# Kernel tuning notes

Measured on AMD Instinct MI355X. Metric: run time of the kernel, lower is better.

Reference implementation:

```python
import jax, jax.numpy as jnp
import numpy as np

N_NODES = 50000
N_EDGES = 400000
N_GRAPHS = 256
NUM_TYPES = 200
EMB = 64
HID = 128
HEADS = 4
GDIM = 256  # graph_embed_dim
NUM_CLASSES = 20
EPS = 1e-5
NEG_SLOPE = 0.2


def _gat_conv(h, src, dst, W, a_src, a_dst, bias, heads, out_c, concat):
    """PyG GATConv (with self-loops already appended to src/dst)."""
    n = h.shape[0]
    x = (h @ W.T).reshape(n, heads, out_c)                       # [N,H,C]
    al_s = jnp.einsum('nhc,hc->nh', x, a_src)                    # [N,H]
    al_d = jnp.einsum('nhc,hc->nh', x, a_dst)
    e = jax.nn.leaky_relu(al_s[src] + al_d[dst], NEG_SLOPE)      # [E',H]
    # segment softmax over destination node
    e_max = jax.ops.segment_max(e, dst, num_segments=n)
    e_exp = jnp.exp(e - e_max[dst])
    denom = jax.ops.segment_sum(e_exp, dst, num_segments=n)
    alpha = e_exp / denom[dst]                                   # [E',H]
    out = jax.ops.segment_sum(alpha[:, :, None] * x[src], dst, num_segments=n)  # [N,H,C]
    out = out.reshape(n, heads * out_c) if concat else out.mean(axis=1)
    return out + bias


def _batchnorm(h, gamma, beta):
    # training-mode BatchNorm1d over node dim (biased variance, as torch)
    m = h.mean(axis=0)
    v = jnp.mean((h - m) ** 2, axis=0)
    return (h - m) * jax.lax.rsqrt(v + EPS) * gamma + beta


def setup_inputs() -> dict:
    key = jax.random.key(0)
    ks = jax.random.split(key, 32)
    s = 0.1
    inp = {
        'x': jax.random.randint(ks[0], (N_NODES,), 0, NUM_TYPES),
        'edge_index': jax.random.randint(ks[1], (2, N_EDGES), 0, N_NODES),
        'depth': jax.random.uniform(ks[2], (N_NODES,), jnp.float32),
        'batch': jnp.sort(jax.random.randint(ks[3], (N_NODES,), 0, N_GRAPHS)),
        'emb_table': jax.random.normal(ks[4], (NUM_TYPES, EMB), jnp.float32) * s,
        'depth_w': jax.random.normal(ks[5], (EMB, 1), jnp.float32) * s,
        'depth_b': jnp.zeros((EMB,), jnp.float32),
        'W0': jax.random.normal(ks[6], (HEADS * HID, EMB), jnp.float32) * s,
        'as0': jax.random.normal(ks[7], (HEADS, HID), jnp.float32) * s,
        'ad0': jax.random.normal(ks[8], (HEADS, HID), jnp.float32) * s,
        'b0': jnp.zeros((HEADS * HID,), jnp.float32),
        'g0': jnp.ones((HEADS * HID,), jnp.float32),
        'be0': jnp.zeros((HEADS * HID,), jnp.float32),
        'W1': jax.random.normal(ks[9], (HEADS * HID, HEADS * HID), jnp.float32) * s,
        'as1': jax.random.normal(ks[10], (HEADS, HID), jnp.float32) * s,
        'ad1': jax.random.normal(ks[11], (HEADS, HID), jnp.float32) * s,
        'b1': jnp.zeros((HEADS * HID,), jnp.float32),
        'g1': jnp.ones((HEADS * HID,), jnp.float32),
        'be1': jnp.zeros((HEADS * HID,), jnp.float32),
        # layer 2: 512 -> 128, 1 head, no concat
        'W2': jax.random.normal(ks[12], (GDIM // 2, HEADS * HID), jnp.float32) * s,
        'as2': jax.random.normal(ks[13], (1, GDIM // 2), jnp.float32) * s,
        'ad2': jax.random.normal(ks[14], (1, GDIM // 2), jnp.float32) * s,
        'b2': jnp.zeros((GDIM // 2,), jnp.float32),
        'g2': jnp.ones((GDIM // 2,), jnp.float32),
        'be2': jnp.zeros((GDIM // 2,), jnp.float32),
        # classifier: 256 -> 256 -> 20
        'cw1': jax.random.normal(ks[15], (GDIM, 2 * (GDIM // 2)), jnp.float32) * s,
        'cb1': jnp.zeros((GDIM,), jnp.float32),
        'cw2': jax.random.normal(ks[16], (NUM_CLASSES, GDIM), jnp.float32) * s,
        'cb2': jnp.zeros((NUM_CLASSES,), jnp.float32),
    }
    return inp


def reference(x, edge_index, depth, batch, emb_table, depth_w, depth_b,
              W0, as0, ad0, b0, g0, be0,
              W1, as1, ad1, b1, g1, be1,
              W2, as2, ad2, b2, g2, be2,
              cw1, cb1, cw2, cb2):
    n = x.shape[0]
    # node features: type embedding + depth projection
    h = emb_table[x] + (depth[:, None] @ depth_w.T + depth_b)    # [N,64]
    # add self-loops once (PyG GATConv default add_self_loops=True)
    loop = jnp.arange(n)
    src = jnp.concatenate([edge_index[0], loop])
    dst = jnp.concatenate([edge_index[1], loop])
    layers = [
        (W0, as0, ad0, b0, g0, be0, HEADS, HID, True),
        (W1, as1, ad1, b1, g1, be1, HEADS, HID, True),
        (W2, as2, ad2, b2, g2, be2, 1, GDIM // 2, False),
    ]
    for (W, a_s, a_d, b, g, be, heads, out_c, concat) in layers:
        h = _gat_conv(h, src, dst, W, a_s, a_d, b, heads, out_c, concat)
        h = _batchnorm(h, g, be)
        h = jax.nn.elu(h)
        # dropout: eval mode -> identity
    # global mean / max pooling per graph
    ones = jnp.ones((n,), h.dtype)
    counts = jax.ops.segment_sum(ones, batch, num_segments=N_GRAPHS)
    h_mean = jax.ops.segment_sum(h, batch, num_segments=N_GRAPHS) / jnp.maximum(counts, 1.0)[:, None]
    h_max = jax.ops.segment_max(h, batch, num_segments=N_GRAPHS)
    emb = jnp.concatenate([h_mean, h_max], axis=-1)              # [G,256]
    # classifier (dropout off in eval)
    hidden = jax.nn.relu(emb @ cw1.T + cb1)
    return hidden @ cw2.T + cb2                                  # [G,20]
```

## Files before the change

### kernel.cpp

```cpp
#include <hip/hip_runtime.h>

#define N_NODES 50000
#define N_PAD 50048
#define NBY 391
#define N_EDGES 400000
#define EP (N_EDGES + N_NODES)
#define N_GRAPHS 256
#define EMB 64
#define HID 128
#define HEADS 4
#define GDIM 256
#define NUM_CLASSES 20
#define EPS_BN 1e-5f
#define NEG_SLOPE 0.2f
#define NB_AGG 2048

typedef __attribute__((ext_vector_type(4))) float f32x4;
typedef _Float16 h8 __attribute__((ext_vector_type(8)));
typedef _Float16 h4 __attribute__((ext_vector_type(4)));
typedef _Float16 h2 __attribute__((ext_vector_type(2)));

#define GLD(g, l)                                                              \
    __builtin_amdgcn_global_load_lds(                                          \
        (const __attribute__((address_space(1))) void*)(g),                    \
        (__attribute__((address_space(3))) void*)(l), 16, 0, 0)

__global__ void k_deg(const int* __restrict__ ei, int* __restrict__ deg) {
    int e = blockIdx.x * blockDim.x + threadIdx.x;
    if (e >= EP) return;
    int dst = (e < N_EDGES) ? ei[N_EDGES + e] : (e - N_EDGES);
    atomicAdd(&deg[dst], 1);
}

__global__ void k_scanA(const int* __restrict__ deg, int* __restrict__ incl, int* __restrict__ bsums) {
    __shared__ int sh[1024];
    int t = threadIdx.x;
    int i = blockIdx.x * 1024 + t;
    int v = (i < N_NODES) ? deg[i] : 0;
    int xv = v;
    sh[t] = xv;
    __syncthreads();
    for (int off = 1; off < 1024; off <<= 1) {
        int y = (t >= off) ? sh[t - off] : 0;
        __syncthreads();
        xv += y;
        sh[t] = xv;
        __syncthreads();
    }
    if (i < N_NODES) incl[i] = xv;
    if (t == 1023) bsums[blockIdx.x] = xv;
}

__global__ void k_scanC(const int* __restrict__ incl, const int* __restrict__ deg,
                        const int* __restrict__ bsums, int* __restrict__ offs) {
    int i = blockIdx.x * blockDim.x + threadIdx.x;
    int b = i >> 10;
    int add = 0;
    for (int k = 0; k < b; k++) add += bsums[k];
    if (i < N_NODES) offs[i] = incl[i] - deg[i] + add;
    if (i == 0) offs[N_NODES] = EP;
}

__global__ void k_scatter(const int* __restrict__ ei, const int* __restrict__ offs,
                          int* __restrict__ cnt, int* __restrict__ csr) {
    int e = blockIdx.x * blockDim.x + threadIdx.x;
    if (e >= EP) return;
    int src, dst;
    if (e < N_EDGES) { src = ei[e]; dst = ei[N_EDGES + e]; }
    else { src = e - N_EDGES; dst = src; }
    int pos = atomicAdd(&cnt[dst], 1);
    csr[offs[dst] + pos] = src;
}

__device__ __forceinline__ void cvt1(const float* __restrict__ in, _Float16* __restrict__ o, int i) {
    int f = i * 4;
    float4 v = *(const float4*)(in + f);
    h4 r;
    r[0] = (_Float16)v.x; r[1] = (_Float16)v.y; r[2] = (_Float16)v.z; r[3] = (_Float16)v.w;
    *(h4*)(o + f) = r;
}

__global__ __launch_bounds__(256) void k_setup(const float* __restrict__ W0, const float* __restrict__ as0,
                                               const float* __restrict__ ad0, const float* __restrict__ W1,
                                               const float* __restrict__ W2,
                                               _Float16* __restrict__ W0f, _Float16* __restrict__ W1f,
                                               _Float16* __restrict__ W2f,
                                               float* __restrict__ wtil,
                                               float* __restrict__ bn0, float* __restrict__ bn1,
                                               float* __restrict__ bn2) {
    int b = blockIdx.x, t = threadIdx.x;
    if (b < 256) {
        cvt1(W1, W1f, b * 256 + t);
    } else if (b < 288) {
        cvt1(W0, W0f, (b - 256) * 256 + t);
    } else if (b < 352) {
        cvt1(W2, W2f, (b - 288) * 256 + t);
    } else if (b == 352) {
        int h = t >> 6, k = t & 63;
        float ss = 0.f, sd = 0.f;
        for (int c = 0; c < 128; c++) {
            float w = W0[(size_t)(h * 128 + c) * 64 + k];
            ss += w * as0[h * 128 + c];
            sd += w * ad0[h * 128 + c];
        }
        wtil[t] = ss;
        wtil[256 + t] = sd;
    } else {
        for (int i = t; i < 1024; i += 256) { bn0[i] = 0.f; bn1[i] = 0.f; bn2[i] = 0.f; }
    }
}

__global__ __launch_bounds__(256) void k_node_al0(const int* __restrict__ x,
                                                  const float* __restrict__ depth,
                                                  const float* __restrict__ emb_table,
                                                  const float* __restrict__ dw,
                                                  const float* __restrict__ db,
                                                  const float* __restrict__ wtil,
                                                  const int* __restrict__ batch,
                                                  _Float16* __restrict__ h16,
                                                  float* __restrict__ als, float* __restrict__ ald,
                                                  int* __restrict__ goffs) {
    int wid = threadIdx.x >> 6, lane = threadIdx.x & 63;
    int n = blockIdx.x * 4 + wid;
    if (n >= N_NODES) return;
    float v = emb_table[x[n] * EMB + lane] + depth[n] * dw[lane] + db[lane];
    h16[(size_t)n * 64 + lane] = (_Float16)v;
#pragma unroll
    for (int h = 0; h < 4; h++) {
        float ps = v * wtil[h * 64 + lane];
        float pd = v * wtil[256 + h * 64 + lane];
        for (int off = 32; off; off >>= 1) {
            ps += __shfl_xor(ps, off);
            pd += __shfl_xor(pd, off);
        }
        if (lane == 0) { als[n * 4 + h] = ps; ald[n * 4 + h] = pd; }
    }
    if (lane == 0) {
        int b = batch[n];
        int bp = (n == 0) ? -1 : batch[n - 1];
        for (int g = bp + 1; g <= b; g++) goffs[g] = n;
        if (n == N_NODES - 1) {
            for (int g = b + 1; g <= N_GRAPHS; g++) goffs[g] = N_NODES;
        }
    }
}

__global__ __launch_bounds__(256) void k_bnelu(_Float16* __restrict__ a,
                                               const float* __restrict__ sums,
                                               const float* __restrict__ gamma,
                                               const float* __restrict__ beta) {
    const int lane = threadIdx.x & 63;
    const int wid = threadIdx.x >> 6;
    const int c0 = lane * 8;
    const float invN = 1.f / (float)N_NODES;
    float sc[8], sh[8];
#pragma unroll
    for (int k = 0; k < 8; k += 4) {
        float4 s4 = *(const float4*)(sums + c0 + k);
        float4 q4 = *(const float4*)(sums + 512 + c0 + k);
        float4 g4 = *(const float4*)(gamma + c0 + k);
        float4 b4 = *(const float4*)(beta + c0 + k);
        float m, v;
        m = s4.x * invN; v = q4.x * invN - m * m;
        sc[k + 0] = g4.x * __frsqrt_rn(v + EPS_BN); sh[k + 0] = b4.x - m * sc[k + 0];
        m = s4.y * invN; v = q4.y * invN - m * m;
        sc[k + 1] = g4.y * __frsqrt_rn(v + EPS_BN); sh[k + 1] = b4.y - m * sc[k + 1];
        m = s4.z * invN; v = q4.z * invN - m * m;
        sc[k + 2] = g4.z * __frsqrt_rn(v + EPS_BN); sh[k + 2] = b4.z - m * sc[k + 2];
        m = s4.w * invN; v = q4.w * invN - m * m;
        sc[k + 3] = g4.w * __frsqrt_rn(v + EPS_BN); sh[k + 3] = b4.w - m * sc[k + 3];
    }
    const int stride = gridDim.x * 8;
    for (int n = (blockIdx.x * 4 + wid) * 2; n < N_NODES; n += stride) {
        _Float16* p0 = a + (size_t)n * 512 + c0;
        _Float16* p1 = p0 + 512;
        h8 v0 = *(h8*)p0;
        h8 v1 = *(h8*)p1;
        h8 o0, o1;
#pragma unroll
        for (int k = 0; k < 8; k++) {
            float x0 = (float)v0[k] * sc[k] + sh[k];
            x0 = x0 > 0.f ? x0 : expm1f(x0);
            o0[k] = (_Float16)x0;
            float x1 = (float)v1[k] * sc[k] + sh[k];
            x1 = x1 > 0.f ? x1 : expm1f(x1);
            o1[k] = (_Float16)x1;
        }
        *(h8*)p0 = o0;
        *(h8*)p1 = o1;
    }
}

__global__ __launch_bounds__(256) void k_agg0(const _Float16* __restrict__ h16,
                                              const float* __restrict__ als,
                                              const float* __restrict__ ald_g,
                                              const int* __restrict__ offs,
                                              const int* __restrict__ csr,
                                              _Float16* __restrict__ outh) {
    const int lane = threadIdx.x & 63;
    const int wwid = threadIdx.x >> 6;
    const int q = lane >> 4, l = lane & 15;
    const int gw = blockIdx.x * 4 + wwid;
    const int stride = gridDim.x * 16;
    for (int n = gw * 4 + q; n < N_NODES; n += stride) {
        int s0 = offs[n], s1 = offs[n + 1];
        float aldl = (l < 4) ? ald_g[n * 4 + l] : 0.f;
        float acc[4][4] = {};
        float den[4] = {};
        int e = s0;
        for (; e + 4 <= s1; e += 4) {
            int srcA = csr[e], srcB = csr[e + 1];
            int srcC = csr[e + 2], srcD = csr[e + 3];
            float wA = 0.f, wB = 0.f, wC = 0.f, wD = 0.f;
            if (l < 4) {
                float a1 = als[srcA * 4 + l] + aldl;
                a1 = a1 > 0.f ? a1 : NEG_SLOPE * a1;
                wA = expf(a1);
                float a2 = als[srcB * 4 + l] + aldl;
                a2 = a2 > 0.f ? a2 : NEG_SLOPE * a2;
                wB = expf(a2);
                float a3 = als[srcC * 4 + l] + aldl;
                a3 = a3 > 0.f ? a3 : NEG_SLOPE * a3;
                wC = expf(a3);
                float a4 = als[srcD * 4 + l] + aldl;
                a4 = a4 > 0.f ? a4 : NEG_SLOPE * a4;
                wD = expf(a4);
            }
            h4 vA = *(const h4*)(h16 + (size_t)srcA * 64 + l * 4);
            h4 vB = *(const h4*)(h16 + (size_t)srcB * 64 + l * 4);
            h4 vC = *(const h4*)(h16 + (size_t)srcC * 64 + l * 4);
            h4 vD = *(const h4*)(h16 + (size_t)srcD * 64 + l * 4);
            float vA0 = (float)vA[0], vA1 = (float)vA[1], vA2 = (float)vA[2], vA3 = (float)vA[3];
            float vB0 = (float)vB[0], vB1 = (float)vB[1], vB2 = (float)vB[2], vB3 = (float)vB[3];
            float vC0 = (float)vC[0], vC1 = (float)vC[1], vC2 = (float)vC[2], vC3 = (float)vC[3];
            float vD0 = (float)vD[0], vD1 = (float)vD[1], vD2 = (float)vD[2], vD3 = (float)vD[3];
#pragma unroll
            for (int h = 0; h < 4; h++) {
                float whA = __shfl(wA, q * 16 + h);
                float whB = __shfl(wB, q * 16 + h);
                float whC = __shfl(wC, q * 16 + h);
                float whD = __shfl(wD, q * 16 + h);
                den[h] += (whA + whB) + (whC + whD);
                acc[h][0] += whA * vA0 + whB * vB0 + whC * vC0 + whD * vD0;
                acc[h][1] += whA * vA1 + whB * vB1 + whC * vC1 + whD * vD1;
                acc[h][2] += whA * vA2 + whB * vB2 + whC * vC2 + whD * vD2;
                acc[h][3] += whA * vA3 + whB * vB3 + whC * vC3 + whD * vD3;
            }
        }
        for (; e < s1; e++) {
            int src = csr[e];
            float w = 0.f;
            if (l < 4) {
                float a1 = als[src * 4 + l] + aldl;
                a1 = a1 > 0.f ? a1 : NEG_SLOPE * a1;
                w = expf(a1);
            }
            h4 v = *(const h4*)(h16 + (size_t)src * 64 + l * 4);
            float v0 = (float)v[0], v1 = (float)v[1], v2 = (float)v[2], v3 = (float)v[3];
#pragma unroll
            for (int h = 0; h < 4; h++) {
                float wh = __shfl(w, q * 16 + h);
                den[h] += wh;
                acc[h][0] += wh * v0;
                acc[h][1] += wh * v1;
                acc[h][2] += wh * v2;
                acc[h][3] += wh * v3;
            }
        }
#pragma unroll
        for (int h = 0; h < 4; h++) {
            float id = 1.f / den[h];
            h4 hv;
            hv[0] = (_Float16)(acc[h][0] * id);
            hv[1] = (_Float16)(acc[h][1] * id);
            hv[2] = (_Float16)(acc[h][2] * id);
            hv[3] = (_Float16)(acc[h][3] * id);
            *(h4*)(outh + (size_t)n * 256 + h * 64 + l * 4) = hv;
        }
    }
}

__global__ __launch_bounds__(256) void k_gemm0h(const _Float16* __restrict__ A,
                                                const _Float16* __restrict__ W,
                                                const float* __restrict__ bias,
                                                _Float16* __restrict__ outA,
                                                float* __restrict__ bnacc) {
    __shared__ h8 sA[2][512], sW[2][512];
    const int nbx = gridDim.x;
    const int d = blockIdx.y * nbx + blockIdx.x;
    const int by = (d / (8 * nbx)) * 8 + (d & 7);
    const int bx = (d >> 3) % nbx;
    if (by >= NBY) return;
    const int hd = bx;
    const int t = threadIdx.x;
    const int lane = t & 63;
    const int wid = t >> 6;
    const int wm = wid >> 1, wn = wid & 1;
    const int r0 = by * 128;
    const int l15 = lane & 15, quad = lane >> 4;
    f32x4 acc[4][4] = {};
    auto stage = [&](int buf, int kb) {
#pragma unroll
        for (int r = 0; r < 2; r++) {
            int c = r * 256 + t;
            int row = c >> 2, q = c & 3;
            size_t gA = ((size_t)(r0 + row) * 256 + hd * 64 + kb) * 2 + q * 16;
            size_t gW = ((size_t)(hd * 128 + row) * 64 + kb) * 2 + q * 16;
            GLD((const char*)A + gA, (char*)&sA[buf][0] + c * 16);
            GLD((const char*)W + gW, (char*)&sW[buf][0] + c * 16);
        }
    };
    stage(0, 0);
    __syncthreads();
#pragma unroll
    for (int ki = 0; ki < 2; ki++) {
        int cur = ki & 1;
        if (ki + 1 < 2) stage(cur ^ 1, (ki + 1) * 32);
        h8 a[4], w[4];
#pragma unroll
        for (int i = 0; i < 4; i++) {
            a[i] = sA[cur][(wm * 64 + i * 16 + l15) * 4 + quad];
            w[i] = sW[cur][(wn * 64 + i * 16 + l15) * 4 + quad];
        }
#pragma unroll
        for (int i = 0; i < 4; i++)
#pragma unroll
            for (int j = 0; j < 4; j++)
                acc[i][j] = __builtin_amdgcn_mfma_f32_16x16x32_f16(a[i], w[j], acc[i][j], 0, 0, 0);
        __syncthreads();
    }
    float colsum[4] = {}, colsq[4] = {};
#pragma unroll
    for (int i = 0; i < 4; i++) {
        int gr = r0 + wm * 64 + i * 16 + quad * 4;
#pragma unroll
        for (int j = 0; j < 4; j++) {
            int gc = hd * 128 + wn * 64 + j * 16 + l15;
            float bv = bias[gc];
#pragma unroll
            for (int rg = 0; rg < 4; rg++) {
                int rr = gr + rg;
                if (rr < N_NODES) {
                    float o = acc[i][j][rg] + bv;
                    outA[(size_t)rr * 512 + gc] = (_Float16)o;
                    colsum[j] += o;
                    colsq[j] += o * o;
                }
            }
        }
    }
#pragma unroll
    for (int j = 0; j < 4; j++) {
        colsum[j] += __shfl_xor(colsum[j], 16);
        colsum[j] += __shfl_xor(colsum[j], 32);
        colsq[j] += __shfl_xor(colsq[j], 16);
        colsq[j] += __shfl_xor(colsq[j], 32);
    }
    float* sS = (float*)&sA[0][0];
    float* sQ = (float*)&sW[0][0];
    __syncthreads();
    if (quad == 0) {
#pragma unroll
        for (int j = 0; j < 4; j++) {
            int c = wn * 64 + j * 16 + l15;
            sS[c * 2 + wm] = colsum[j];
            sQ[c * 2 + wm] = colsq[j];
        }
    }
    __syncthreads();
    if (t < 128) {
        atomicAdd(bnacc + hd * 128 + t, sS[t * 2] + sS[t * 2 + 1]);
        atomicAdd(bnacc + 512 + hd * 128 + t, sQ[t * 2] + sQ[t * 2 + 1]);
    }
}

__global__ __launch_bounds__(256) void k_gemm_mfma(const _Float16* __restrict__ A,
                                                   const _Float16* __restrict__ W,
                                                   const float* __restrict__ a_src,
                                                   const float* __restrict__ a_dst,
                                                   float* __restrict__ als_g,
                                                   float* __restrict__ ald_g,
                                                   _Float16* __restrict__ out,
                                                   int K, int M, int heads) {
    __shared__ h8 sA[2][512], sW[2][512];
    const int nbx = gridDim.x;
    const int d = blockIdx.y * nbx + blockIdx.x;
    const int by = (d / (8 * nbx)) * 8 + (d & 7);
    const int bx = (d >> 3) % nbx;
    if (by >= NBY) return;
    const int t = threadIdx.x;
    const int lane = t & 63;
    const int wid = t >> 6;
    const int wm = wid >> 1, wn = wid & 1;
    const int r0 = by * 128, c0 = bx * 128;
    const int l15 = lane & 15, quad = lane >> 4;
    f32x4 acc[4][4] = {};
    auto stage = [&](int buf, int kb) {
#pragma unroll
        for (int r = 0; r < 2; r++) {
            int c = r * 256 + t;
            int row = c >> 2, q = c & 3;
            size_t gA = ((size_t)(r0 + row) * K + kb) * 2 + q * 16;
            size_t gW = ((size_t)(c0 + row) * K + kb) * 2 + q * 16;
            GLD((const char*)A + gA, (char*)&sA[buf][0] + c * 16);
            GLD((const char*)W + gW, (char*)&sW[buf][0] + c * 16);
        }
    };
    stage(0, 0);
    __syncthreads();
    const int nkb = K >> 5;
    for (int ki = 0; ki < nkb; ki++) {
        int cur = ki & 1;
        if (ki + 1 < nkb) stage(cur ^ 1, (ki + 1) * 32);
        h8 a[4], w[4];
#pragma unroll
        for (int i = 0; i < 4; i++) {
            a[i] = sA[cur][(wm * 64 + i * 16 + l15) * 4 + quad];
            w[i] = sW[cur][(wn * 64 + i * 16 + l15) * 4 + quad];
        }
#pragma unroll
        for (int i = 0; i < 4; i++)
#pragma unroll
            for (int j = 0; j < 4; j++)
                acc[i][j] = __builtin_amdgcn_mfma_f32_16x16x32_f16(a[i], w[j], acc[i][j], 0, 0, 0);
        __syncthreads();
    }
#pragma unroll
    for (int i = 0; i < 4; i++) {
        int gr = r0 + wm * 64 + i * 16 + quad * 4;
#pragma unroll
        for (int j = 0; j < 4; j++) {
            int gc = c0 + wn * 64 + j * 16 + l15;
#pragma unroll
            for (int rg = 0; rg < 4; rg++) {
                int rr = gr + rg;
                if (rr < N_NODES) out[(size_t)rr * M + gc] = (_Float16)acc[i][j][rg];
            }
        }
    }
    const int hd = bx;
    float ps[4][4] = {}, pd[4][4] = {};
#pragma unroll
    for (int j = 0; j < 4; j++) {
        int ch = wn * 64 + j * 16 + l15;
        float av = a_src[hd * 128 + ch];
        float dv = a_dst[hd * 128 + ch];
#pragma unroll
        for (int i = 0; i < 4; i++)
#pragma unroll
            for (int rg = 0; rg < 4; rg++) {
                ps[i][rg] += acc[i][j][rg] * av;
                pd[i][rg] += acc[i][j][rg] * dv;
            }
    }
#pragma unroll
    for (int m = 1; m < 16; m <<= 1)
#pragma unroll
        for (int i = 0; i < 4; i++)
#pragma unroll
            for (int rg = 0; rg < 4; rg++) {
                ps[i][rg] += __shfl_xor(ps[i][rg], m);
                pd[i][rg] += __shfl_xor(pd[i][rg], m);
            }
    float* sS = (float*)&sA[0][0];
    float* sD = (float*)&sW[0][0];
    if (l15 == 0) {
#pragma unroll
        for (int i = 0; i < 4; i++)
#pragma unroll
            for (int rg = 0; rg < 4; rg++) {
                int ri = wm * 64 + i * 16 + quad * 4 + rg;
                sS[ri * 2 + wn] = ps[i][rg];
                sD[ri * 2 + wn] = pd[i][rg];
            }
    }
    __syncthreads();
    if (t < 128) {
        int row = r0 + t;
        if (row < N_NODES) {
            als_g[row * heads + hd] = sS[t * 2] + sS[t * 2 + 1];
            ald_g[row * heads + hd] = sD[t * 2] + sD[t * 2 + 1];
        }
    }
}

__global__ __launch_bounds__(256) void k_agg512(const _Float16* __restrict__ xf,
                                                const float* __restrict__ als,
                                                const float* __restrict__ ald_g,
                                                const int* __restrict__ offs,
                                                const int* __restrict__ csr,
                                                const float* __restrict__ bias,
                                                _Float16* __restrict__ out16,
                                                float* __restrict__ bnacc) {
    __shared__ float pool[4][1024];
    const int wid = threadIdx.x >> 6, lane = threadIdx.x & 63;
    int* s_src = (int*)&pool[wid][0];
    float* s_w = &pool[wid][64];
    const int gw = blockIdx.x * 4 + wid;
    const int nw = gridDim.x * 4;
    const int hh = lane >> 4;
    const int c0 = lane * 8;
    float bias8[8];
#pragma unroll
    for (int k = 0; k < 8; k++) bias8[k] = bias[c0 + k];
    float bns[8] = {}, bnq[8] = {};
    for (int n = gw; n < N_NODES; n += nw) {
        int s0 = offs[n], s1 = offs[n + 1];
        float4 aldv = *(const float4*)(ald_g + n * 4);
        float a[8] = {};
        float den = 0.f;
        for (int base = s0; base < s1; base += 64) {
            int j = base + lane;
            int srcj = 0;
            float4 alv = make_float4(0.f, 0.f, 0.f, 0.f);
            if (j < s1) {
                srcj = csr[j];
                alv = *(const float4*)(als + srcj * 4);
            }
            float e0 = alv.x + aldv.x; e0 = e0 > 0.f ? e0 : NEG_SLOPE * e0;
            float e1 = alv.y + aldv.y; e1 = e1 > 0.f ? e1 : NEG_SLOPE * e1;
            float e2 = alv.z + aldv.z; e2 = e2 > 0.f ? e2 : NEG_SLOPE * e2;
            float e3 = alv.w + aldv.w; e3 = e3 > 0.f ? e3 : NEG_SLOPE * e3;
            s_src[lane] = srcj;
            s_w[0 * 64 + lane] = expf(e0);
            s_w[1 * 64 + lane] = expf(e1);
            s_w[2 * 64 + lane] = expf(e2);
            s_w[3 * 64 + lane] = expf(e3);
            int cend = min(64, s1 - base);
            int e = 0;
            for (; e + 8 <= cend; e += 8) {
                h8 v[8];
                float w[8];
#pragma unroll
                for (int u = 0; u < 8; u++) {
                    v[u] = *(const h8*)(xf + (size_t)s_src[e + u] * 512 + c0);
                    w[u] = s_w[hh * 64 + e + u];
                }
#pragma unroll
                for (int u = 0; u < 8; u++) {
                    den += w[u];
#pragma unroll
                    for (int k = 0; k < 8; k++) a[k] += w[u] * (float)v[u][k];
                }
            }
            for (; e + 2 <= cend; e += 2) {
                h8 vA = *(const h8*)(xf + (size_t)s_src[e] * 512 + c0);
                h8 vB = *(const h8*)(xf + (size_t)s_src[e + 1] * 512 + c0);
                float wA = s_w[hh * 64 + e], wB = s_w[hh * 64 + e + 1];
                den += wA + wB;
#pragma unroll
                for (int k = 0; k < 8; k++) a[k] += wA * (float)vA[k] + wB * (float)vB[k];
            }
            if (e < cend) {
                h8 v = *(const h8*)(xf + (size_t)s_src[e] * 512 + c0);
                float w = s_w[hh * 64 + e];
                den += w;
#pragma unroll
                for (int k = 0; k < 8; k++) a[k] += w * (float)v[k];
            }
        }
        float id = 1.f / den;
        h8 ov;
#pragma unroll
        for (int k = 0; k < 8; k++) {
            float o = a[k] * id + bias8[k];
            ov[k] = (_Float16)o;
            bns[k] += o;
            bnq[k] += o * o;
        }
        *(h8*)(out16 + (size_t)n * 512 + c0) = ov;
    }
#pragma unroll
    for (int k = 0; k < 8; k++) {
        pool[wid][c0 + k] = bns[k];
        pool[wid][512 + c0 + k] = bnq[k];
    }
    __syncthreads();
    for (int t = threadIdx.x; t < 1024; t += 256)
        atomicAdd(bnacc + t, pool[0][t] + pool[1][t] + pool[2][t] + pool[3][t]);
}

__global__ __launch_bounds__(256) void k_agg128(const _Float16* __restrict__ xf,
                                                const float* __restrict__ als,
                                                const float* __restrict__ ald_g,
                                                const int* __restrict__ offs,
                                                const int* __restrict__ csr,
                                                const float* __restrict__ bias,
                                                _Float16* __restrict__ out_h,
                                                float* __restrict__ bnacc) {
    __shared__ float pool[4][256];
    const int wid = threadIdx.x >> 6, lane = threadIdx.x & 63;
    int* s_src = (int*)&pool[wid][0];
    float* s_w = &pool[wid][64];
    const int gw = blockIdx.x * 4 + wid;
    const int nw = gridDim.x * 4;
    const int c = lane * 2;
    const float2 biasv = *(const float2*)(bias + c);
    float bns0 = 0.f, bns1 = 0.f, bnq0 = 0.f, bnq1 = 0.f;
    for (int n = gw; n < N_NODES; n += nw) {
        int s0 = offs[n], s1 = offs[n + 1];
        float aldv = ald_g[n];
        float ax = 0.f, ay = 0.f, den = 0.f;
        for (int base = s0; base < s1; base += 64) {
            int j = base + lane;
            int srcj = 0;
            float alv = 0.f;
            if (j < s1) { srcj = csr[j]; alv = als[srcj]; }
            float e0 = alv + aldv;
            e0 = e0 > 0.f ? e0 : NEG_SLOPE * e0;
            s_src[lane] = srcj;
            s_w[lane] = expf(e0);
            int cend = min(64, s1 - base);
            int e = 0;
            for (; e + 8 <= cend; e += 8) {
                h2 v[8];
                float w[8];
#pragma unroll
                for (int u = 0; u < 8; u++) {
                    v[u] = *(const h2*)(xf + (size_t)s_src[e + u] * 128 + c);
                    w[u] = s_w[e + u];
                }
#pragma unroll
                for (int u = 0; u < 8; u++) {
                    den += w[u];
                    ax += w[u] * (float)v[u][0];
                    ay += w[u] * (float)v[u][1];
                }
            }
            for (; e < cend; e++) {
                h2 v = *(const h2*)(xf + (size_t)s_src[e] * 128 + c);
                float w = s_w[e];
                den += w;
                ax += w * (float)v[0];
                ay += w * (float)v[1];
            }
        }
        float id = 1.f / den;
        float ox = ax * id + biasv.x;
        float oy = ay * id + biasv.y;
        h2 oh;
        oh[0] = (_Float16)ox;
        oh[1] = (_Float16)oy;
        *(h2*)(out_h + (size_t)n * 128 + c) = oh;
        bns0 += ox; bnq0 += ox * ox;
        bns1 += oy; bnq1 += oy * oy;
    }
    pool[wid][c] = bns0; pool[wid][c + 1] = bns1;
    pool[wid][128 + c] = bnq0; pool[wid][128 + c + 1] = bnq1;
    __syncthreads();
    {
        int t = threadIdx.x;
        atomicAdd(bnacc + t, pool[0][t] + pool[1][t] + pool[2][t] + pool[3][t]);
    }
}

__global__ __launch_bounds__(256) void k_poolclassify(const _Float16* __restrict__ C,
                                                      const float* __restrict__ bnsums,
                                                      const float* __restrict__ gamma,
                                                      const float* __restrict__ beta,
                                                      const int* __restrict__ goffs,
                                                      const float* __restrict__ cw1, const float* __restrict__ cb1,
                                                      const float* __restrict__ cw2, const float* __restrict__ cb2,
                                                      float* __restrict__ out) {
    __shared__ float er[256];
    __shared__ float red[256];
    int g = blockIdx.x, t = threadIdx.x;
    int c = t & 127, half = t >> 7;
    const float invN = 1.f / (float)N_NODES;
    float m = bnsums[c] * invN;
    float var = bnsums[128 + c] * invN - m * m;
    float sc = gamma[c] * __frsqrt_rn(var + EPS_BN);
    float sh = beta[c] - m * sc;
    int s = goffs[g], e = goffs[g + 1];
    float sum = 0.f, mx = -INFINITY;
    for (int n = s + half; n < e; n += 2) {
        float x = (float)C[(size_t)n * 128 + c] * sc + sh;
        x = x > 0.f ? x : expm1f(x);
        sum += x;
        mx = fmaxf(mx, x);
    }
    red[t] = sum;
    __syncthreads();
    float sumT = red[c] + red[128 + c];
    __syncthreads();
    red[t] = mx;
    __syncthreads();
    float mxT = fmaxf(red[c], red[128 + c]);
    int cnt = e - s;
    if (half == 0) {
        er[c] = sumT / (float)max(cnt, 1);
        er[128 + c] = mxT;
    }
    __syncthreads();
    float acc = cb1[t];
    for (int k = 0; k < 256; k++) acc += er[k] * cw1[t * 256 + k];
    __syncthreads();
    red[t] = fmaxf(acc, 0.f);
    __syncthreads();
    if (t < NUM_CLASSES) {
        float o = cb2[t];
        for (int k = 0; k < 256; k++) o += red[k] * cw2[t * 256 + k];
        out[g * NUM_CLASSES + t] = o;
    }
}

extern "C" void kernel_launch(void* const* d_in, const int* in_sizes, int n_in,
                              void* d_out, int out_size, void* d_ws, size_t ws_size,
                              hipStream_t stream) {
    (void)in_sizes; (void)n_in; (void)out_size; (void)ws_size;
    const int* x = (const int*)d_in[0];
    const int* ei = (const int*)d_in[1];
    const float* depth = (const float*)d_in[2];
    const int* batch = (const int*)d_in[3];
    const float* emb_table = (const float*)d_in[4];
    const float* depth_w = (const float*)d_in[5];
    const float* depth_b = (const float*)d_in[6];
    const float* W0 = (const float*)d_in[7];
    const float* as0 = (const float*)d_in[8];
    const float* ad0 = (const float*)d_in[9];
    const float* b0 = (const float*)d_in[10];
    const float* g0 = (const float*)d_in[11];
    const float* be0 = (const float*)d_in[12];
    const float* W1 = (const float*)d_in[13];
    const float* as1 = (const float*)d_in[14];
    const float* ad1 = (const float*)d_in[15];
    const float* b1 = (const float*)d_in[16];
    const float* g1 = (const float*)d_in[17];
    const float* be1 = (const float*)d_in[18];
    const float* W2 = (const float*)d_in[19];
    const float* as2 = (const float*)d_in[20];
    const float* ad2 = (const float*)d_in[21];
    const float* b2 = (const float*)d_in[22];
    const float* g2 = (const float*)d_in[23];
    const float* be2 = (const float*)d_in[24];
    const float* cw1 = (const float*)d_in[25];
    const float* cb1 = (const float*)d_in[26];
    const float* cw2 = (const float*)d_in[27];
    const float* cb2 = (const float*)d_in[28];
    float* out = (float*)d_out;

    size_t off = 0;
    char* base = (char*)d_ws;
    auto carve = [&](size_t bytes) -> void* {
        void* p = base + off;
        off += (bytes + 255) & ~(size_t)255;
        return p;
    };
    float* B = (float*)carve((size_t)N_NODES * 512 * 2);
    _Float16* A16 = (_Float16*)carve((size_t)N_PAD * 512 * 2);
    _Float16* W0f = (_Float16*)carve((size_t)512 * 64 * 2);
    _Float16* W1f = (_Float16*)carve((size_t)512 * 512 * 2);
    _Float16* W2f = (_Float16*)carve((size_t)128 * 512 * 2);
    float* als = (float*)carve((size_t)N_NODES * HEADS * 4);
    float* ald = (float*)carve((size_t)N_NODES * HEADS * 4);
    float* bn0 = (float*)carve(1024 * 4);
    float* bn1 = (float*)carve(1024 * 4);
    float* bn2 = (float*)carve(1024 * 4);
    float* wtil = (float*)carve(512 * 4);
    int* deg = (int*)carve((size_t)2 * N_NODES * 4);
    int* cnt = deg + N_NODES;
    int* incl = (int*)carve((size_t)N_NODES * 4);
    int* offs = (int*)carve((size_t)(N_NODES + 1) * 4);
    int* bsums = (int*)carve(64 * 4);
    int* csr = (int*)carve((size_t)EP * 4);
    int* goffs = (int*)carve((size_t)(N_GRAPHS + 1) * 4);

    _Float16* h16 = (_Float16*)B;
    _Float16* hth = (_Float16*)((char*)B + (size_t)N_NODES * 64 * 2);
    _Float16* Bh = (_Float16*)B;
    _Float16* C = (_Float16*)A16;

    const int TPB = 256;
    int gbN = (N_NODES + TPB - 1) / TPB;
    int gbE = (EP + TPB - 1) / TPB;
    int nbScan = (N_NODES + 1023) / 1024;
    int gbNode4 = (N_NODES + 3) / 4;
    dim3 g512(4, 392);
    dim3 g128(1, 391);

    hipMemsetAsync(deg, 0, (size_t)2 * N_NODES * 4, stream);
    k_setup<<<354, TPB, 0, stream>>>(W0, as0, ad0, W1, W2, W0f, W1f, W2f, wtil, bn0, bn1, bn2);
    k_deg<<<gbE, TPB, 0, stream>>>(ei, deg);
    k_scanA<<<nbScan, 1024, 0, stream>>>(deg, incl, bsums);
    k_scanC<<<gbN, TPB, 0, stream>>>(incl, deg, bsums, offs);
    k_scatter<<<gbE, TPB, 0, stream>>>(ei, offs, cnt, csr);

    k_node_al0<<<gbNode4, TPB, 0, stream>>>(x, depth, emb_table, depth_w, depth_b, wtil,
                                            batch, h16, als, ald, goffs);
    k_agg0<<<NB_AGG, TPB, 0, stream>>>(h16, als, ald, offs, csr, hth);
    k_gemm0h<<<g512, TPB, 0, stream>>>(hth, W0f, b0, A16, bn0);
    k_bnelu<<<2048, TPB, 0, stream>>>(A16, bn0, g0, be0);
    k_gemm_mfma<<<g512, TPB, 0, stream>>>(A16, W1f, as1, ad1, als, ald, Bh, 512, 512, HEADS);
    k_agg512<<<NB_AGG, TPB, 0, stream>>>(Bh, als, ald, offs, csr, b1, A16, bn1);
    k_bnelu<<<2048, TPB, 0, stream>>>(A16, bn1, g1, be1);
    k_gemm_mfma<<<g128, TPB, 0, stream>>>(A16, W2f, as2, ad2, als, ald, Bh, 512, 128, 1);
    k_agg128<<<NB_AGG, TPB, 0, stream>>>(Bh, als, ald, offs, csr, b2, C, bn2);
    k_poolclassify<<<N_GRAPHS, TPB, 0, stream>>>(C, bn2, g2, be2, goffs, cw1, cb1, cw2, cb2, out);
}
```

Measured before the change: 581.4 us.

## Fuse BatchNorm+ELU into GEMM A-tile staging and fold deg memset into setup

Removes the two standalone BN+ELU passes over the 50000x512 fp16 activations. The BN scale and shift are now computed per block into shared memory, and the normalisation and ELU are applied while the A tile is loaded through registers into LDS inside the MFMA GEMM. A is loaded with register loads instead of async global-to-LDS loads, and the transform is interleaved after the MFMAs. The deg/cnt memset is folded into extra blocks of the setup kernel. The cost is that the ELU is recomputed for every column block (4x for layer 1) and the A load path is no longer asynchronous.

```diff
diff --git a/kernel.cpp b/kernel.cpp
--- a/kernel.cpp
+++ b/kernel.cpp
@@ -87,7 +87,8 @@
                                                _Float16* __restrict__ W2f,
                                                float* __restrict__ wtil,
                                                float* __restrict__ bn0, float* __restrict__ bn1,
-                                               float* __restrict__ bn2) {
+                                               float* __restrict__ bn2,
+                                               int* __restrict__ deg) {
     int b = blockIdx.x, t = threadIdx.x;
     if (b < 256) {
         cvt1(W1, W1f, b * 256 + t);
@@ -105,8 +106,11 @@
         }
         wtil[t] = ss;
         wtil[256 + t] = sd;
+    } else if (b == 353) {
+        for (int i = t; i < 1024; i += 256) { bn0[i] = 0.f; bn1[i] = 0.f; bn2[i] = 0.f; }
     } else {
-        for (int i = t; i < 1024; i += 256) { bn0[i] = 0.f; bn1[i] = 0.f; bn2[i] = 0.f; }
+        int i4 = (b - 354) * 256 + t;
+        if (i4 < 25000) ((int4*)deg)[i4] = make_int4(0, 0, 0, 0);
     }
 }
 
@@ -142,52 +146,6 @@
         if (n == N_NODES - 1) {
             for (int g = b + 1; g <= N_GRAPHS; g++) goffs[g] = N_NODES;
         }
-    }
-}
-
-__global__ __launch_bounds__(256) void k_bnelu(_Float16* __restrict__ a,
-                                               const float* __restrict__ sums,
-                                               const float* __restrict__ gamma,
-                                               const float* __restrict__ beta) {
-    const int lane = threadIdx.x & 63;
-    const int wid = threadIdx.x >> 6;
-    const int c0 = lane * 8;
-    const float invN = 1.f / (float)N_NODES;
-    float sc[8], sh[8];
-#pragma unroll
-    for (int k = 0; k < 8; k += 4) {
-        float4 s4 = *(const float4*)(sums + c0 + k);
-        float4 q4 = *(const float4*)(sums + 512 + c0 + k);
-        float4 g4 = *(const float4*)(gamma + c0 + k);
-        float4 b4 = *(const float4*)(beta + c0 + k);
-        float m, v;
-        m = s4.x * invN; v = q4.x * invN - m * m;
-        sc[k + 0] = g4.x * __frsqrt_rn(v + EPS_BN); sh[k + 0] = b4.x - m * sc[k + 0];
-        m = s4.y * invN; v = q4.y * invN - m * m;
-        sc[k + 1] = g4.y * __frsqrt_rn(v + EPS_BN); sh[k + 1] = b4.y - m * sc[k + 1];
-        m = s4.z * invN; v = q4.z * invN - m * m;
-        sc[k + 2] = g4.z * __frsqrt_rn(v + EPS_BN); sh[k + 2] = b4.z - m * sc[k + 2];
-        m = s4.w * invN; v = q4.w * invN - m * m;
-        sc[k + 3] = g4.w * __frsqrt_rn(v + EPS_BN); sh[k + 3] = b4.w - m * sc[k + 3];
-    }
-    const int stride = gridDim.x * 8;
-    for (int n = (blockIdx.x * 4 + wid) * 2; n < N_NODES; n += stride) {
-        _Float16* p0 = a + (size_t)n * 512 + c0;
-        _Float16* p1 = p0 + 512;
-        h8 v0 = *(h8*)p0;
-        h8 v1 = *(h8*)p1;
-        h8 o0, o1;
-#pragma unroll
-        for (int k = 0; k < 8; k++) {
-            float x0 = (float)v0[k] * sc[k] + sh[k];
-            x0 = x0 > 0.f ? x0 : expm1f(x0);
-            o0[k] = (_Float16)x0;
-            float x1 = (float)v1[k] * sc[k] + sh[k];
-            x1 = x1 > 0.f ? x1 : expm1f(x1);
-            o1[k] = (_Float16)x1;
-        }
-        *(h8*)p0 = o0;
-        *(h8*)p1 = o1;
     }
 }
 
@@ -376,6 +334,9 @@
 
 __global__ __launch_bounds__(256) void k_gemm_mfma(const _Float16* __restrict__ A,
                                                    const _Float16* __restrict__ W,
+                                                   const float* __restrict__ bnsums,
+                                                   const float* __restrict__ gamma,
+                                                   const float* __restrict__ beta,
                                                    const float* __restrict__ a_src,
                                                    const float* __restrict__ a_dst,
                                                    float* __restrict__ als_g,
@@ -383,6 +344,7 @@
                                                    _Float16* __restrict__ out,
                                                    int K, int M, int heads) {
     __shared__ h8 sA[2][512], sW[2][512];
+    __shared__ float sSC[512], sSH[512];
     const int nbx = gridDim.x;
     const int d = blockIdx.y * nbx + blockIdx.x;
     const int by = (d / (8 * nbx)) * 8 + (d & 7);
@@ -395,23 +357,69 @@
     const int r0 = by * 128, c0 = bx * 128;
     const int l15 = lane & 15, quad = lane >> 4;
     f32x4 acc[4][4] = {};
-    auto stage = [&](int buf, int kb) {
+    {
+        const float invN = 1.f / (float)N_NODES;
+        for (int c = t; c < 512; c += 256) {
+            float m = bnsums[c] * invN;
+            float var = bnsums[512 + c] * invN - m * m;
+            float s = gamma[c] * __frsqrt_rn(var + EPS_BN);
+            sSC[c] = s;
+            sSH[c] = beta[c] - m * s;
+        }
+    }
+    auto stageW = [&](int buf, int kb) {
 #pragma unroll
         for (int r = 0; r < 2; r++) {
             int c = r * 256 + t;
             int row = c >> 2, q = c & 3;
-            size_t gA = ((size_t)(r0 + row) * K + kb) * 2 + q * 16;
             size_t gW = ((size_t)(c0 + row) * K + kb) * 2 + q * 16;
-            GLD((const char*)A + gA, (char*)&sA[buf][0] + c * 16);
             GLD((const char*)W + gW, (char*)&sW[buf][0] + c * 16);
         }
     };
-    stage(0, 0);
+    auto loadA = [&](int kb, h8* va) {
+#pragma unroll
+        for (int r = 0; r < 2; r++) {
+            int c = r * 256 + t;
+            int row = c >> 2, q = c & 3;
+            va[r] = *(const h8*)(A + (size_t)(r0 + row) * K + kb + q * 8);
+        }
+    };
+    auto writeA = [&](int buf, int kb, const h8* va) {
+#pragma unroll
+        for (int r = 0; r < 2; r++) {
+            int c = r * 256 + t;
+            int q = c & 3;
+            int col = kb + q * 8;
+            float4 c0v = *(const float4*)&sSC[col];
+            float4 c1v = *(const float4*)&sSC[col + 4];
+            float4 h0v = *(const float4*)&sSH[col];
+            float4 h1v = *(const float4*)&sSH[col + 4];
+            h8 o;
+            float x;
+            x = (float)va[r][0] * c0v.x + h0v.x; x = x > 0.f ? x : expm1f(x); o[0] = (_Float16)x;
+            x = (float)va[r][1] * c0v.y + h0v.y; x = x > 0.f ? x : expm1f(x); o[1] = (_Float16)x;
+            x = (float)va[r][2] * c0v.z + h0v.z; x = x > 0.f ? x : expm1f(x); o[2] = (_Float16)x;
+            x = (float)va[r][3] * c0v.w + h0v.w; x = x > 0.f ? x : expm1f(x); o[3] = (_Float16)x;
+            x = (float)va[r][4] * c1v.x + h1v.x; x = x > 0.f ? x : expm1f(x); o[4] = (_Float16)x;
+            x = (float)va[r][5] * c1v.y + h1v.y; x = x > 0.f ? x : expm1f(x); o[5] = (_Float16)x;
+            x = (float)va[r][6] * c1v.z + h1v.z; x = x > 0.f ? x : expm1f(x); o[6] = (_Float16)x;
+            x = (float)va[r][7] * c1v.w + h1v.w; x = x > 0.f ? x : expm1f(x); o[7] = (_Float16)x;
+            sA[buf][c] = o;
+        }
+    };
+    h8 va[2];
+    loadA(0, va);
+    stageW(0, 0);
+    __syncthreads();
+    writeA(0, 0, va);
     __syncthreads();
     const int nkb = K >> 5;
     for (int ki = 0; ki < nkb; ki++) {
         int cur = ki & 1;
-        if (ki + 1 < nkb) stage(cur ^ 1, (ki + 1) * 32);
+        if (ki + 1 < nkb) {
+            loadA((ki + 1) * 32, va);
+            stageW(cur ^ 1, (ki + 1) * 32);
+        }
         h8 a[4], w[4];
 #pragma unroll
         for (int i = 0; i < 4; i++) {
@@ -423,6 +431,7 @@
 #pragma unroll
             for (int j = 0; j < 4; j++)
                 acc[i][j] = __builtin_amdgcn_mfma_f32_16x16x32_f16(a[i], w[j], acc[i][j], 0, 0, 0);
+        if (ki + 1 < nkb) writeA(cur ^ 1, (ki + 1) * 32, va);
         __syncthreads();
     }
 #pragma unroll
@@ -778,8 +787,8 @@
     dim3 g512(4, 392);
     dim3 g128(1, 391);
 
-    hipMemsetAsync(deg, 0, (size_t)2 * N_NODES * 4, stream);
-    k_setup<<<354, TPB, 0, stream>>>(W0, as0, ad0, W1, W2, W0f, W1f, W2f, wtil, bn0, bn1, bn2);
+    k_setup<<<452, TPB, 0, stream>>>(W0, as0, ad0, W1, W2, W0f, W1f, W2f, wtil,
+                                     bn0, bn1, bn2, deg);
     k_deg<<<gbE, TPB, 0, stream>>>(ei, deg);
     k_scanA<<<nbScan, 1024, 0, stream>>>(deg, incl, bsums);
     k_scanC<<<gbN, TPB, 0, stream>>>(incl, deg, bsums, offs);
@@ -789,11 +798,9 @@
                                             batch, h16, als, ald, goffs);
     k_agg0<<<NB_AGG, TPB, 0, stream>>>(h16, als, ald, offs, csr, hth);
     k_gemm0h<<<g512, TPB, 0, stream>>>(hth, W0f, b0, A16, bn0);
-    k_bnelu<<<2048, TPB, 0, stream>>>(A16, bn0, g0, be0);
-    k_gemm_mfma<<<g512, TPB, 0, stream>>>(A16, W1f, as1, ad1, als, ald, Bh, 512, 512, HEADS);
+    k_gemm_mfma<<<g512, TPB, 0, stream>>>(A16, W1f, bn0, g0, be0, as1, ad1, als, ald, Bh, 512, 512, HEADS);
     k_agg512<<<NB_AGG, TPB, 0, stream>>>(Bh, als, ald, offs, csr, b1, A16, bn1);
-    k_bnelu<<<2048, TPB, 0, stream>>>(A16, bn1, g1, be1);
-    k_gemm_mfma<<<g128, TPB, 0, stream>>>(A16, W2f, as2, ad2, als, ald, Bh, 512, 128, 1);
+    k_gemm_mfma<<<g128, TPB, 0, stream>>>(A16, W2f, bn1, g1, be1, as2, ad2, als, ald, Bh, 512, 128, 1);
     k_agg128<<<NB_AGG, TPB, 0, stream>>>(Bh, als, ald, offs, csr, b2, C, bn2);
     k_poolclassify<<<N_GRAPHS, TPB, 0, stream>>>(C, bn2, g2, be2, goffs, cw1, cb1, cw2, cb2, out);
 }
```

Measured after the change: 620.9 us. +6.8%, slower.
